# Optimization experiments

Measured on AMD Instinct MI355X. Metric: run time of the kernel, lower is better.

Reference implementation:

```python
import jax, jax.numpy as jnp
import numpy as np

ROWS, CELLS = 64, 64          # B table rows, C cells per row
CN_LEN, CV_LEN = 8, 16        # tokens per column name / cell value
EMB, HID = 768, 3072
VOCAB, NTYPES = 32000, 8
N = ROWS * CELLS              # total cells
L_CV = CELLS * CV_LEN         # padded per-row cv length (max possible)


def setup_inputs() -> dict:
    key = jax.random.key(0)
    ks = jax.random.split(key, 12)
    cn_ids = jax.random.randint(ks[0], (N, CN_LEN), 0, VOCAB)
    # guarantee at least one valid token per column name (avoid div by zero)
    cn_mask = jax.random.randint(ks[1], (N, CN_LEN), 0, 2).at[:, 0].set(1)
    c_types = jax.random.randint(ks[2], (N,), 0, NTYPES)
    cv_ids = jax.random.randint(ks[3], (N, CV_LEN), 0, VOCAB)
    cv_mask = jax.random.randint(ks[4], (N, CV_LEN), 0, 2).astype(bool)
    s = 1.0 / np.sqrt(EMB)
    word_emb = jax.random.normal(ks[5], (VOCAB, EMB), jnp.float32) * 0.02
    type_emb = jax.random.normal(ks[6], (NTYPES, EMB), jnp.float32) * 0.02
    fuse_w1 = jax.random.normal(ks[7], (EMB, HID), jnp.float32) * s
    fuse_b1 = jnp.zeros((HID,), jnp.float32)
    fuse_w2 = jax.random.normal(ks[8], (HID, 1), jnp.float32) / np.sqrt(HID)
    fuse_b2 = jnp.zeros((1,), jnp.float32)
    gate_w1 = jax.random.normal(ks[9], (EMB, HID), jnp.float32) * s
    gate_b1 = jnp.zeros((HID,), jnp.float32)
    gate_w2 = jax.random.normal(ks[10], (HID, 1), jnp.float32) / np.sqrt(HID)
    gate_b2 = jnp.zeros((1,), jnp.float32)
    cls_weight = jax.random.uniform(ks[11], (1, 1, EMB), jnp.float32, -s, s)
    return dict(cn_ids=cn_ids, cn_mask=cn_mask, c_types=c_types, cv_ids=cv_ids,
                cv_mask=cv_mask, word_emb=word_emb, type_emb=type_emb,
                fuse_w1=fuse_w1, fuse_b1=fuse_b1, fuse_w2=fuse_w2, fuse_b2=fuse_b2,
                gate_w1=gate_w1, gate_b1=gate_b1, gate_w2=gate_w2, gate_b2=gate_b2,
                cls_weight=cls_weight)


def reference(cn_ids, cn_mask, c_types, cv_ids, cv_mask, word_emb, type_emb,
              fuse_w1, fuse_b1, fuse_w2, fuse_b2, gate_w1, gate_b1, gate_w2,
              gate_b2, cls_weight):
    # --- TabColumnEmb: masked avg of column-name tokens + datatype gate ---
    cn_we = word_emb[cn_ids]                                  # [N, cn_len, E]
    m = cn_mask.astype(cn_we.dtype)
    cn_e = (cn_we * m[..., None]).sum(1) / m.sum(1, keepdims=True)  # [N, E]
    dt_e = type_emb[c_types]                                  # [N, E]
    fgate = jax.nn.sigmoid(jax.nn.relu(dt_e @ fuse_w1 + fuse_b1) @ fuse_w2 + fuse_b2)
    cn_e = cn_e + dt_e * fgate
    # --- TabColumnValueEmb + RelationLink ---
    cv_e = word_emb[cv_ids]                                   # [N, cv_len, E]
    g = jax.nn.sigmoid(jax.nn.relu(cn_e @ gate_w1 + gate_b1) @ gate_w2 + gate_b2)
    linked = cv_e + (cn_e * g)[:, None, :]                    # [N, cv_len, E]
    # --- per-row ragged gather of masked cv tokens, zero-padded to L_CV ---
    cn_rows = cn_e.reshape(ROWS, CELLS, EMB)
    cv_rows = linked.reshape(ROWS, L_CV, EMB)
    mrows = cv_mask.reshape(ROWS, L_CV)
    pos = jnp.clip(jnp.cumsum(mrows.astype(jnp.int32), axis=1) - 1, 0, L_CV - 1)
    bidx = jnp.arange(ROWS)[:, None]
    mf = mrows[..., None].astype(cv_rows.dtype)
    # masked-out tokens contribute exact zeros -> pad_zeros semantics preserved
    cv_out = jnp.zeros((ROWS, L_CV, EMB), cv_rows.dtype).at[bidx, pos].add(cv_rows * mf)
    # --- TabCLSEmb: prepend learnable cls token ---
    cls = jnp.broadcast_to(cls_weight, (ROWS, 1, EMB))
    return jnp.concatenate([cls, cn_rows, cv_out], axis=1)    # [B, 1+C+L_CV, E]
```

## Files before the change

### kernel.cpp

```cpp
#include <hip/hip_runtime.h>
#include <hip/hip_bf16.h>

#define ROWS 64
#define CELLS 64
#define CN_LEN 8
#define CV_LEN 16
#define EMB 768
#define HID 3072
#define NCELL 4096
#define L_CV 1024
#define ROW_TOK 1089
#define HBLK 24

#define OFF_FPART 0UL
#define OFF_FGATE (OFF_FPART + 96UL*8*4)
#define OFF_GPART (OFF_FGATE + 64UL)
#define OFF_CNB   (OFF_GPART + 24UL*4096*4)
#define OFF_W1T   (OFF_CNB + 4096UL*768*2)
#define OFF_CST   (OFF_W1T + 3072UL*768*2)
#define OFF_CNT   (OFF_CST + 4096UL*4)

typedef __attribute__((ext_vector_type(8))) short bf16x8;
typedef __attribute__((ext_vector_type(4))) float f32x4;

static __device__ __forceinline__ short f2bf(float x) {
  unsigned u = __float_as_uint(x);
  unsigned r = (u + 0x7fffu + ((u >> 16) & 1u)) >> 16;
  return (short)r;
}

static __device__ __forceinline__ void gload16(const void* g, void* l) {
  __builtin_amdgcn_global_load_lds(
      (const __attribute__((address_space(1))) unsigned*)g,
      (__attribute__((address_space(3))) unsigned*)l, 16, 0, 0);
}

__global__ __launch_bounds__(512) void k_fgate_acc(
    const float* __restrict__ type_emb, const float* __restrict__ fuse_w1,
    const float* __restrict__ fuse_b1, const float* __restrict__ fuse_w2,
    float* __restrict__ fpart) {
  __shared__ float te[8 * EMB];
  __shared__ float red[16][8][33];
  const int tid = threadIdx.x;
  for (int i = tid; i < 8 * EMB; i += 512) te[i] = type_emb[i];
  __syncthreads();
  const int hl = tid & 31, eg = tid >> 5;
  const int h = blockIdx.x * 32 + hl;
  float acc[8] = {0.f, 0.f, 0.f, 0.f, 0.f, 0.f, 0.f, 0.f};
  const float* wp = fuse_w1 + h;
  #pragma unroll 4
  for (int i = 0; i < 48; i++) {
    const int e = eg * 48 + i;
    const float wv = wp[(size_t)e * HID];
    #pragma unroll
    for (int t = 0; t < 8; t++) acc[t] += te[t * EMB + e] * wv;
  }
  #pragma unroll
  for (int t = 0; t < 8; t++) red[eg][t][hl] = acc[t];
  __syncthreads();
  if (tid < 256) {
    const int t = tid >> 5, h2 = tid & 31;
    float a = fuse_b1[blockIdx.x * 32 + h2];
    #pragma unroll
    for (int e2 = 0; e2 < 16; e2++) a += red[e2][t][h2];
    float v = fmaxf(a, 0.f) * fuse_w2[blockIdx.x * 32 + h2];
    #pragma unroll
    for (int m = 1; m < 32; m <<= 1) v += __shfl_xor(v, m);
    if (h2 == 0) fpart[blockIdx.x * 8 + t] = v;
  }
}

__global__ __launch_bounds__(256) void k_w1t(const float* __restrict__ w1,
                                             short* __restrict__ w1t,
                                             const float* __restrict__ fpart,
                                             const float* __restrict__ fuse_b2,
                                             float* __restrict__ fgate) {
  __shared__ float tile[32][33];
  const int bx = blockIdx.x, by = blockIdx.y;
  const int tid = threadIdx.x;
  if (bx == 0 && by == 0 && tid < 8) {
    float s = fuse_b2[0];
    for (int j = 0; j < 96; j++) s += fpart[j * 8 + tid];
    fgate[tid] = 1.f / (1.f + expf(-s));
  }
  #pragma unroll
  for (int i = 0; i < 4; i++) {
    int idx = tid + i * 256;
    int rr = idx >> 5, cc = idx & 31;
    tile[rr][cc] = w1[(size_t)(by * 32 + rr) * HID + bx * 32 + cc];
  }
  __syncthreads();
  #pragma unroll
  for (int i = 0; i < 4; i++) {
    int idx = tid + i * 256;
    int rr = idx >> 5, cc = idx & 31;
    w1t[(size_t)(bx * 32 + rr) * EMB + by * 32 + cc] = f2bf(tile[cc][rr]);
  }
}

__global__ __launch_bounds__(192) void k_cn(
    const int* __restrict__ cn_ids, const int* __restrict__ cn_mask,
    const int* __restrict__ c_types, const float* __restrict__ word_emb,
    const float* __restrict__ type_emb, const float* __restrict__ cls_w,
    const float* __restrict__ fgate, short* __restrict__ cnb,
    float* __restrict__ out) {
  const int n = blockIdx.x, tid = threadIdx.x;
  const int row = n >> 6, cell = n & 63;
  const int* ids = cn_ids + n * CN_LEN;
  const int* msk = cn_mask + n * CN_LEN;
  float4 s = {0.f, 0.f, 0.f, 0.f};
  int cnt = 0;
  #pragma unroll
  for (int j = 0; j < CN_LEN; j++) {
    if (msk[j]) {
      cnt++;
      const float4 v = *(const float4*)&word_emb[(size_t)ids[j] * EMB + tid * 4];
      s.x += v.x; s.y += v.y; s.z += v.z; s.w += v.w;
    }
  }
  const float inv = 1.f / (float)cnt;
  const int t = c_types[n];
  const float fg = fgate[t];
  const float4 d = *(const float4*)&type_emb[(size_t)t * EMB + tid * 4];
  float4 c;
  c.x = s.x * inv + d.x * fg;
  c.y = s.y * inv + d.y * fg;
  c.z = s.z * inv + d.z * fg;
  c.w = s.w * inv + d.w * fg;
  short4 b;
  b.x = f2bf(c.x); b.y = f2bf(c.y); b.z = f2bf(c.z); b.w = f2bf(c.w);
  *(short4*)&cnb[(size_t)n * EMB + tid * 4] = b;
  *(float4*)&out[(size_t)row * ROW_TOK * EMB + (size_t)(1 + cell) * EMB + tid * 4] = c;
  if (cell == 0)
    *(float4*)&out[(size_t)row * ROW_TOK * EMB + tid * 4] =
        *(const float4*)&cls_w[tid * 4];
}

__global__ __launch_bounds__(512) void k_gate_gemm(
    const short* __restrict__ cnb, const short* __restrict__ w1t,
    const float* __restrict__ gate_b1, const float* __restrict__ gate_w2,
    float* __restrict__ gpart) {
  __shared__ short Asub[256 * 32];
  __shared__ short Bsub[128 * 32];
  const int tid = threadIdx.x;
  const int n0 = blockIdx.x * 256;
  const int h0 = blockIdx.y * 128;
  const int lane = tid & 63, w = tid >> 6;
  const int wr = w >> 1, wc = w & 1;
  const int r = lane & 15, g = lane >> 4;
  f32x4 acc[4][4];
  #pragma unroll
  for (int a = 0; a < 4; a++)
    #pragma unroll
    for (int b = 0; b < 4; b++) acc[a][b] = (f32x4)0.f;

  const int s0 = tid, s1 = tid + 512;
  const int ar0 = s0 >> 2, ac0 = (s0 & 3) * 8;
  const int ar1 = s1 >> 2, ac1 = (s1 & 3) * 8;

  for (int kk = 0; kk < EMB; kk += 32) {
    gload16(cnb + (size_t)(n0 + ar0) * EMB + kk + ac0, Asub + s0 * 8);
    gload16(cnb + (size_t)(n0 + ar1) * EMB + kk + ac1, Asub + s1 * 8);
    gload16(w1t + (size_t)(h0 + ar0) * EMB + kk + ac0, Bsub + s0 * 8);
    __syncthreads();
    bf16x8 fa[4], fb[4];
    #pragma unroll
    for (int fm = 0; fm < 4; fm++)
      fa[fm] = *(const bf16x8*)&Asub[(wr * 64 + fm * 16 + r) * 32 + g * 8];
    #pragma unroll
    for (int fn = 0; fn < 4; fn++)
      fb[fn] = *(const bf16x8*)&Bsub[(wc * 64 + fn * 16 + r) * 32 + g * 8];
    #pragma unroll
    for (int fm = 0; fm < 4; fm++)
      #pragma unroll
      for (int fn = 0; fn < 4; fn++)
        acc[fm][fn] = __builtin_amdgcn_mfma_f32_16x16x32_bf16(
            fa[fm], fb[fn], acc[fm][fn], 0, 0, 0);
    __syncthreads();
  }

  float rsum[4][4];
  #pragma unroll
  for (int fm = 0; fm < 4; fm++) {
    float rs[4] = {0.f, 0.f, 0.f, 0.f};
    #pragma unroll
    for (int fn = 0; fn < 4; fn++) {
      const int h = h0 + wc * 64 + fn * 16 + r;
      const float bv = gate_b1[h];
      const float wv = gate_w2[h];
      #pragma unroll
      for (int q = 0; q < 4; q++)
        rs[q] += fmaxf(acc[fm][fn][q] + bv, 0.f) * wv;
    }
    #pragma unroll
    for (int q = 0; q < 4; q++) {
      #pragma unroll
      for (int m = 1; m < 16; m <<= 1) rs[q] += __shfl_xor(rs[q], m);
      rsum[fm][q] = rs[q];
    }
  }
  float* red = (float*)Asub;
  __syncthreads();
  if (wc == 1 && r == 0) {
    #pragma unroll
    for (int fm = 0; fm < 4; fm++)
      #pragma unroll
      for (int q = 0; q < 4; q++)
        red[wr * 64 + fm * 16 + g * 4 + q] = rsum[fm][q];
  }
  __syncthreads();
  if (wc == 0 && r == 0) {
    #pragma unroll
    for (int fm = 0; fm < 4; fm++)
      #pragma unroll
      for (int q = 0; q < 4; q++) {
        const int i = wr * 64 + fm * 16 + g * 4 + q;
        gpart[(size_t)blockIdx.y * NCELL + n0 + i] = rsum[fm][q] + red[i];
      }
  }
}

__global__ __launch_bounds__(256) void k_prefix(const int* __restrict__ cv_mask,
                                                int* __restrict__ cstart,
                                                int* __restrict__ cnt) {
  const int row = blockIdx.x, tid = threadIdx.x;
  __shared__ int ssum[256];
  int m[4];
  const int base = row * L_CV + tid * 4;
  int s = 0;
  #pragma unroll
  for (int i = 0; i < 4; i++) { m[i] = cv_mask[base + i]; s += m[i]; }
  ssum[tid] = s;
  __syncthreads();
  for (int off = 1; off < 256; off <<= 1) {
    int v = (tid >= off) ? ssum[tid - off] : 0;
    __syncthreads();
    ssum[tid] += v;
    __syncthreads();
  }
  if ((tid & 3) == 0) cstart[row * CELLS + (tid >> 2)] = ssum[tid] - s;
  if (tid == 255) cnt[row] = ssum[255];
}

__global__ __launch_bounds__(192) void k_cv_cell(
    const int* __restrict__ cv_ids, const int* __restrict__ cv_mask,
    const int* __restrict__ cstart, const int* __restrict__ cnt,
    const float* __restrict__ word_emb, const float* __restrict__ gpart,
    const float* __restrict__ gate_b2, float* __restrict__ out) {
  const int bx = blockIdx.x, row = blockIdx.y, tid = threadIdx.x;
  const size_t rbase = (size_t)row * ROW_TOK * EMB;
  if (bx >= CELLS) {
    const int base = cnt[row] + (bx - CELLS) * 8;
    const float4 z = {0.f, 0.f, 0.f, 0.f};
    #pragma unroll
    for (int i = 0; i < 8; i++) {
      const int k = base + i;
      if (k < L_CV)
        *(float4*)&out[rbase + (size_t)(65 + k) * EMB + tid * 4] = z;
    }
    return;
  }
  const int cell = bx;
  const int n = row * CELLS + cell;
  float sg = gate_b2[0];
  #pragma unroll
  for (int j = 0; j < HBLK; j++) sg += gpart[(size_t)j * NCELL + n];
  const float gg = 1.f / (1.f + expf(-sg));
  const float4 cn = *(const float4*)&out[rbase + (size_t)(1 + cell) * EMB + tid * 4];
  float4 cg;
  cg.x = cn.x * gg; cg.y = cn.y * gg; cg.z = cn.z * gg; cg.w = cn.w * gg;
  const int* ids = cv_ids + n * CV_LEN;
  const int* msk = cv_mask + n * CV_LEN;
  int pos = cstart[n];
  #pragma unroll
  for (int j = 0; j < CV_LEN; j++) {
    if (msk[j]) {
      const float4 we = *(const float4*)&word_emb[(size_t)ids[j] * EMB + tid * 4];
      float4 v;
      v.x = we.x + cg.x; v.y = we.y + cg.y; v.z = we.z + cg.z; v.w = we.w + cg.w;
      *(float4*)&out[rbase + (size_t)(65 + pos) * EMB + tid * 4] = v;
      pos++;
    }
  }
}

extern "C" void kernel_launch(void* const* d_in, const int* in_sizes, int n_in,
                              void* d_out, int out_size, void* d_ws, size_t ws_size,
                              hipStream_t stream) {
  const int* cn_ids    = (const int*)d_in[0];
  const int* cn_mask   = (const int*)d_in[1];
  const int* c_types   = (const int*)d_in[2];
  const int* cv_ids    = (const int*)d_in[3];
  const int* cv_mask   = (const int*)d_in[4];
  const float* word_emb = (const float*)d_in[5];
  const float* type_emb = (const float*)d_in[6];
  const float* fuse_w1  = (const float*)d_in[7];
  const float* fuse_b1  = (const float*)d_in[8];
  const float* fuse_w2  = (const float*)d_in[9];
  const float* fuse_b2  = (const float*)d_in[10];
  const float* gate_w1  = (const float*)d_in[11];
  const float* gate_b1  = (const float*)d_in[12];
  const float* gate_w2  = (const float*)d_in[13];
  const float* gate_b2  = (const float*)d_in[14];
  const float* cls_w    = (const float*)d_in[15];

  char* ws = (char*)d_ws;
  float* fpart = (float*)(ws + OFF_FPART);
  float* fgate = (float*)(ws + OFF_FGATE);
  float* gpart = (float*)(ws + OFF_GPART);
  short* cnb   = (short*)(ws + OFF_CNB);
  short* w1t   = (short*)(ws + OFF_W1T);
  int*   cst   = (int*)(ws + OFF_CST);
  int*   cntp  = (int*)(ws + OFF_CNT);
  float* out   = (float*)d_out;

  k_fgate_acc<<<96, 512, 0, stream>>>(type_emb, fuse_w1, fuse_b1, fuse_w2, fpart);
  k_w1t<<<dim3(96, 24), 256, 0, stream>>>(gate_w1, w1t, fpart, fuse_b2, fgate);
  k_cn<<<NCELL, 192, 0, stream>>>(cn_ids, cn_mask, c_types, word_emb, type_emb,
                                  cls_w, fgate, cnb, out);
  k_gate_gemm<<<dim3(16, HBLK), 512, 0, stream>>>(cnb, w1t, gate_b1, gate_w2, gpart);
  k_prefix<<<64, 256, 0, stream>>>(cv_mask, cst, cntp);
  k_cv_cell<<<dim3(CELLS + 128, ROWS), 192, 0, stream>>>(cv_ids, cv_mask, cst,
                                                         cntp, word_emb, gpart,
                                                         gate_b2, out);
}
```

Measured before the change: 125.2 us.

## Double-buffer gate GEMM, retile to 128x128 with XCD remap, fold prefix into fgate

```diff
diff --git a/kernel.cpp b/kernel.cpp
--- a/kernel.cpp
+++ b/kernel.cpp
@@ -38,10 +38,29 @@
 __global__ __launch_bounds__(512) void k_fgate_acc(
     const float* __restrict__ type_emb, const float* __restrict__ fuse_w1,
     const float* __restrict__ fuse_b1, const float* __restrict__ fuse_w2,
-    float* __restrict__ fpart) {
+    float* __restrict__ fpart, const int* __restrict__ cv_mask,
+    int* __restrict__ cstart, int* __restrict__ cnt) {
   __shared__ float te[8 * EMB];
   __shared__ float red[16][8][33];
+  __shared__ int ssum[512];
   const int tid = threadIdx.x;
+  if (blockIdx.x >= 96) {
+    const int row = blockIdx.x - 96;
+    const int base = row * L_CV + tid * 2;
+    const int m0 = cv_mask[base], m1 = cv_mask[base + 1];
+    const int s = m0 + m1;
+    ssum[tid] = s;
+    __syncthreads();
+    for (int off = 1; off < 512; off <<= 1) {
+      int v = (tid >= off) ? ssum[tid - off] : 0;
+      __syncthreads();
+      ssum[tid] += v;
+      __syncthreads();
+    }
+    if ((tid & 7) == 0) cstart[row * CELLS + (tid >> 3)] = ssum[tid] - s;
+    if (tid == 511) cnt[row] = ssum[511];
+    return;
+  }
   for (int i = tid; i < 8 * EMB; i += 512) te[i] = type_emb[i];
   __syncthreads();
   const int hl = tid & 31, eg = tid >> 5;
@@ -136,15 +155,17 @@
         *(const float4*)&cls_w[tid * 4];
 }
 
-__global__ __launch_bounds__(512) void k_gate_gemm(
+__global__ __launch_bounds__(256) void k_gate_gemm(
     const short* __restrict__ cnb, const short* __restrict__ w1t,
     const float* __restrict__ gate_b1, const float* __restrict__ gate_w2,
     float* __restrict__ gpart) {
-  __shared__ short Asub[256 * 32];
-  __shared__ short Bsub[128 * 32];
+  __shared__ short Asub[2][128 * 32];
+  __shared__ short Bsub[2][128 * 32];
   const int tid = threadIdx.x;
-  const int n0 = blockIdx.x * 256;
-  const int h0 = blockIdx.y * 128;
+  const int orig = blockIdx.x;
+  const int wgid = (orig & 7) * 96 + (orig >> 3);
+  const int bx = wgid & 31, by = wgid >> 5;
+  const int n0 = bx * 128, h0 = by * 128;
   const int lane = tid & 63, w = tid >> 6;
   const int wr = w >> 1, wc = w & 1;
   const int r = lane & 15, g = lane >> 4;
@@ -154,30 +175,47 @@
     #pragma unroll
     for (int b = 0; b < 4; b++) acc[a][b] = (f32x4)0.f;
 
-  const int s0 = tid, s1 = tid + 512;
+  const int s0 = tid, s1 = tid + 256;
   const int ar0 = s0 >> 2, ac0 = (s0 & 3) * 8;
   const int ar1 = s1 >> 2, ac1 = (s1 & 3) * 8;
-
-  for (int kk = 0; kk < EMB; kk += 32) {
-    gload16(cnb + (size_t)(n0 + ar0) * EMB + kk + ac0, Asub + s0 * 8);
-    gload16(cnb + (size_t)(n0 + ar1) * EMB + kk + ac1, Asub + s1 * 8);
-    gload16(w1t + (size_t)(h0 + ar0) * EMB + kk + ac0, Bsub + s0 * 8);
+  const short* aB = cnb + (size_t)n0 * EMB;
+  const short* bB = w1t + (size_t)h0 * EMB;
+
+#define STAGE(buf, kk)                                                  \
+  do {                                                                  \
+    gload16(aB + (size_t)ar0 * EMB + (kk) + ac0, &Asub[buf][s0 * 8]);   \
+    gload16(aB + (size_t)ar1 * EMB + (kk) + ac1, &Asub[buf][s1 * 8]);   \
+    gload16(bB + (size_t)ar0 * EMB + (kk) + ac0, &Bsub[buf][s0 * 8]);   \
+    gload16(bB + (size_t)ar1 * EMB + (kk) + ac1, &Bsub[buf][s1 * 8]);   \
+  } while (0)
+
+#define COMPUTE(buf)                                                          \
+  do {                                                                        \
+    bf16x8 fa[4], fb[4];                                                      \
+    _Pragma("unroll")                                                         \
+    for (int fm = 0; fm < 4; fm++)                                            \
+      fa[fm] = *(const bf16x8*)&Asub[buf][(wr * 64 + fm * 16 + r) * 32 + g * 8]; \
+    _Pragma("unroll")                                                         \
+    for (int fn = 0; fn < 4; fn++)                                            \
+      fb[fn] = *(const bf16x8*)&Bsub[buf][(wc * 64 + fn * 16 + r) * 32 + g * 8]; \
+    _Pragma("unroll")                                                         \
+    for (int fm = 0; fm < 4; fm++)                                            \
+      _Pragma("unroll")                                                       \
+      for (int fn = 0; fn < 4; fn++)                                          \
+        acc[fm][fn] = __builtin_amdgcn_mfma_f32_16x16x32_bf16(                \
+            fa[fm], fb[fn], acc[fm][fn], 0, 0, 0);                            \
+  } while (0)
+
+  STAGE(0, 0);
+  __syncthreads();
+  int cur = 0;
+  for (int t = 0; t < 23; t++) {
+    STAGE(cur ^ 1, (t + 1) * 32);
+    COMPUTE(cur);
     __syncthreads();
-    bf16x8 fa[4], fb[4];
-    #pragma unroll
-    for (int fm = 0; fm < 4; fm++)
-      fa[fm] = *(const bf16x8*)&Asub[(wr * 64 + fm * 16 + r) * 32 + g * 8];
-    #pragma unroll
-    for (int fn = 0; fn < 4; fn++)
-      fb[fn] = *(const bf16x8*)&Bsub[(wc * 64 + fn * 16 + r) * 32 + g * 8];
-    #pragma unroll
-    for (int fm = 0; fm < 4; fm++)
-      #pragma unroll
-      for (int fn = 0; fn < 4; fn++)
-        acc[fm][fn] = __builtin_amdgcn_mfma_f32_16x16x32_bf16(
-            fa[fm], fb[fn], acc[fm][fn], 0, 0, 0);
-    __syncthreads();
-  }
+    cur ^= 1;
+  }
+  COMPUTE(cur);
 
   float rsum[4][4];
   #pragma unroll
@@ -199,7 +237,7 @@
       rsum[fm][q] = rs[q];
     }
   }
-  float* red = (float*)Asub;
+  float* red = (float*)&Asub[0][0];
   __syncthreads();
   if (wc == 1 && r == 0) {
     #pragma unroll
@@ -215,31 +253,11 @@
       #pragma unroll
       for (int q = 0; q < 4; q++) {
         const int i = wr * 64 + fm * 16 + g * 4 + q;
-        gpart[(size_t)blockIdx.y * NCELL + n0 + i] = rsum[fm][q] + red[i];
+        gpart[(size_t)by * NCELL + n0 + i] = rsum[fm][q] + red[i];
       }
   }
-}
-
-__global__ __launch_bounds__(256) void k_prefix(const int* __restrict__ cv_mask,
-                                                int* __restrict__ cstart,
-                                                int* __restrict__ cnt) {
-  const int row = blockIdx.x, tid = threadIdx.x;
-  __shared__ int ssum[256];
-  int m[4];
-  const int base = row * L_CV + tid * 4;
-  int s = 0;
-  #pragma unroll
-  for (int i = 0; i < 4; i++) { m[i] = cv_mask[base + i]; s += m[i]; }
-  ssum[tid] = s;
-  __syncthreads();
-  for (int off = 1; off < 256; off <<= 1) {
-    int v = (tid >= off) ? ssum[tid - off] : 0;
-    __syncthreads();
-    ssum[tid] += v;
-    __syncthreads();
-  }
-  if ((tid & 3) == 0) cstart[row * CELLS + (tid >> 2)] = ssum[tid] - s;
-  if (tid == 255) cnt[row] = ssum[255];
+#undef STAGE
+#undef COMPUTE
 }
 
 __global__ __launch_bounds__(192) void k_cv_cell(
@@ -314,12 +332,12 @@
   int*   cntp  = (int*)(ws + OFF_CNT);
   float* out   = (float*)d_out;
 
-  k_fgate_acc<<<96, 512, 0, stream>>>(type_emb, fuse_w1, fuse_b1, fuse_w2, fpart);
+  k_fgate_acc<<<160, 512, 0, stream>>>(type_emb, fuse_w1, fuse_b1, fuse_w2,
+                                       fpart, cv_mask, cst, cntp);
   k_w1t<<<dim3(96, 24), 256, 0, stream>>>(gate_w1, w1t, fpart, fuse_b2, fgate);
   k_cn<<<NCELL, 192, 0, stream>>>(cn_ids, cn_mask, c_types, word_emb, type_emb,
                                   cls_w, fgate, cnb, out);
-  k_gate_gemm<<<dim3(16, HBLK), 512, 0, stream>>>(cnb, w1t, gate_b1, gate_w2, gpart);
-  k_prefix<<<64, 256, 0, stream>>>(cv_mask, cst, cntp);
+  k_gate_gemm<<<768, 256, 0, stream>>>(cnb, w1t, gate_b1, gate_w2, gpart);
   k_cv_cell<<<dim3(CELLS + 128, ROWS), 192, 0, stream>>>(cv_ids, cv_mask, cst,
                                                          cntp, word_emb, gpart,
                                                          gate_b2, out);
```

After: 123.3 us. No clear change (-1.6%).

## Fold prefix scan into fgate kernel, inline fgate sum, retile gate GEMM

Applied to the files above, without the earlier changes.

```diff
diff --git a/kernel.cpp b/kernel.cpp
--- a/kernel.cpp
+++ b/kernel.cpp
@@ -13,8 +13,7 @@
 #define HBLK 24
 
 #define OFF_FPART 0UL
-#define OFF_FGATE (OFF_FPART + 96UL*8*4)
-#define OFF_GPART (OFF_FGATE + 64UL)
+#define OFF_GPART (OFF_FPART + 96UL*8*4)
 #define OFF_CNB   (OFF_GPART + 24UL*4096*4)
 #define OFF_W1T   (OFF_CNB + 4096UL*768*2)
 #define OFF_CST   (OFF_W1T + 3072UL*768*2)
@@ -38,10 +37,29 @@
 __global__ __launch_bounds__(512) void k_fgate_acc(
     const float* __restrict__ type_emb, const float* __restrict__ fuse_w1,
     const float* __restrict__ fuse_b1, const float* __restrict__ fuse_w2,
-    float* __restrict__ fpart) {
+    float* __restrict__ fpart, const int* __restrict__ cv_mask,
+    int* __restrict__ cstart, int* __restrict__ cnt) {
   __shared__ float te[8 * EMB];
   __shared__ float red[16][8][33];
+  __shared__ int ssum[512];
   const int tid = threadIdx.x;
+  if (blockIdx.x >= 96) {
+    const int row = blockIdx.x - 96;
+    const int base = row * L_CV + tid * 2;
+    const int m0 = cv_mask[base], m1 = cv_mask[base + 1];
+    const int s = m0 + m1;
+    ssum[tid] = s;
+    __syncthreads();
+    for (int off = 1; off < 512; off <<= 1) {
+      int v = (tid >= off) ? ssum[tid - off] : 0;
+      __syncthreads();
+      ssum[tid] += v;
+      __syncthreads();
+    }
+    if ((tid & 7) == 0) cstart[row * CELLS + (tid >> 3)] = ssum[tid] - s;
+    if (tid == 511) cnt[row] = ssum[511];
+    return;
+  }
   for (int i = tid; i < 8 * EMB; i += 512) te[i] = type_emb[i];
   __syncthreads();
   const int hl = tid & 31, eg = tid >> 5;
@@ -71,18 +89,10 @@
 }
 
 __global__ __launch_bounds__(256) void k_w1t(const float* __restrict__ w1,
-                                             short* __restrict__ w1t,
-                                             const float* __restrict__ fpart,
-                                             const float* __restrict__ fuse_b2,
-                                             float* __restrict__ fgate) {
+                                             short* __restrict__ w1t) {
   __shared__ float tile[32][33];
   const int bx = blockIdx.x, by = blockIdx.y;
   const int tid = threadIdx.x;
-  if (bx == 0 && by == 0 && tid < 8) {
-    float s = fuse_b2[0];
-    for (int j = 0; j < 96; j++) s += fpart[j * 8 + tid];
-    fgate[tid] = 1.f / (1.f + expf(-s));
-  }
   #pragma unroll
   for (int i = 0; i < 4; i++) {
     int idx = tid + i * 256;
@@ -102,8 +112,8 @@
     const int* __restrict__ cn_ids, const int* __restrict__ cn_mask,
     const int* __restrict__ c_types, const float* __restrict__ word_emb,
     const float* __restrict__ type_emb, const float* __restrict__ cls_w,
-    const float* __restrict__ fgate, short* __restrict__ cnb,
-    float* __restrict__ out) {
+    const float* __restrict__ fpart, const float* __restrict__ fuse_b2,
+    short* __restrict__ cnb, float* __restrict__ out) {
   const int n = blockIdx.x, tid = threadIdx.x;
   const int row = n >> 6, cell = n & 63;
   const int* ids = cn_ids + n * CN_LEN;
@@ -120,7 +130,10 @@
   }
   const float inv = 1.f / (float)cnt;
   const int t = c_types[n];
-  const float fg = fgate[t];
+  float sg = fuse_b2[0];
+  #pragma unroll 8
+  for (int j = 0; j < 96; j++) sg += fpart[j * 8 + t];
+  const float fg = 1.f / (1.f + expf(-sg));
   const float4 d = *(const float4*)&type_emb[(size_t)t * EMB + tid * 4];
   float4 c;
   c.x = s.x * inv + d.x * fg;
@@ -136,42 +149,49 @@
         *(const float4*)&cls_w[tid * 4];
 }
 
-__global__ __launch_bounds__(512) void k_gate_gemm(
+__global__ __launch_bounds__(256) void k_gate_gemm(
     const short* __restrict__ cnb, const short* __restrict__ w1t,
     const float* __restrict__ gate_b1, const float* __restrict__ gate_w2,
     float* __restrict__ gpart) {
   __shared__ short Asub[256 * 32];
   __shared__ short Bsub[128 * 32];
   const int tid = threadIdx.x;
-  const int n0 = blockIdx.x * 256;
-  const int h0 = blockIdx.y * 128;
+  const int orig = blockIdx.x;
+  const int wgid = (orig & 7) * 48 + (orig >> 3);
+  const int bx = wgid & 15, by = wgid >> 4;
+  const int n0 = bx * 256, h0 = by * 128;
   const int lane = tid & 63, w = tid >> 6;
   const int wr = w >> 1, wc = w & 1;
   const int r = lane & 15, g = lane >> 4;
-  f32x4 acc[4][4];
-  #pragma unroll
-  for (int a = 0; a < 4; a++)
+  f32x4 acc[8][4];
+  #pragma unroll
+  for (int a = 0; a < 8; a++)
     #pragma unroll
     for (int b = 0; b < 4; b++) acc[a][b] = (f32x4)0.f;
 
-  const int s0 = tid, s1 = tid + 512;
-  const int ar0 = s0 >> 2, ac0 = (s0 & 3) * 8;
-  const int ar1 = s1 >> 2, ac1 = (s1 & 3) * 8;
+  const int ar = tid >> 2, ac = (tid & 3) * 8;
+  const short* aB = cnb + (size_t)n0 * EMB;
+  const short* bB = w1t + (size_t)h0 * EMB;
 
   for (int kk = 0; kk < EMB; kk += 32) {
-    gload16(cnb + (size_t)(n0 + ar0) * EMB + kk + ac0, Asub + s0 * 8);
-    gload16(cnb + (size_t)(n0 + ar1) * EMB + kk + ac1, Asub + s1 * 8);
-    gload16(w1t + (size_t)(h0 + ar0) * EMB + kk + ac0, Bsub + s0 * 8);
+    #pragma unroll
+    for (int i = 0; i < 4; i++)
+      gload16(aB + (size_t)(ar + i * 64) * EMB + kk + ac,
+              Asub + (ar + i * 64) * 32 + ac);
+    #pragma unroll
+    for (int i = 0; i < 2; i++)
+      gload16(bB + (size_t)(ar + i * 64) * EMB + kk + ac,
+              Bsub + (ar + i * 64) * 32 + ac);
     __syncthreads();
-    bf16x8 fa[4], fb[4];
-    #pragma unroll
-    for (int fm = 0; fm < 4; fm++)
-      fa[fm] = *(const bf16x8*)&Asub[(wr * 64 + fm * 16 + r) * 32 + g * 8];
+    bf16x8 fa[8], fb[4];
+    #pragma unroll
+    for (int fm = 0; fm < 8; fm++)
+      fa[fm] = *(const bf16x8*)&Asub[(wr * 128 + fm * 16 + r) * 32 + g * 8];
     #pragma unroll
     for (int fn = 0; fn < 4; fn++)
       fb[fn] = *(const bf16x8*)&Bsub[(wc * 64 + fn * 16 + r) * 32 + g * 8];
     #pragma unroll
-    for (int fm = 0; fm < 4; fm++)
+    for (int fm = 0; fm < 8; fm++)
       #pragma unroll
       for (int fn = 0; fn < 4; fn++)
         acc[fm][fn] = __builtin_amdgcn_mfma_f32_16x16x32_bf16(
@@ -179,9 +199,9 @@
     __syncthreads();
   }
 
-  float rsum[4][4];
-  #pragma unroll
-  for (int fm = 0; fm < 4; fm++) {
+  float rsum[8][4];
+  #pragma unroll
+  for (int fm = 0; fm < 8; fm++) {
     float rs[4] = {0.f, 0.f, 0.f, 0.f};
     #pragma unroll
     for (int fn = 0; fn < 4; fn++) {
@@ -203,43 +223,21 @@
   __syncthreads();
   if (wc == 1 && r == 0) {
     #pragma unroll
-    for (int fm = 0; fm < 4; fm++)
+    for (int fm = 0; fm < 8; fm++)
       #pragma unroll
       for (int q = 0; q < 4; q++)
-        red[wr * 64 + fm * 16 + g * 4 + q] = rsum[fm][q];
+        red[wr * 128 + fm * 16 + g * 4 + q] = rsum[fm][q];
   }
   __syncthreads();
   if (wc == 0 && r == 0) {
     #pragma unroll
-    for (int fm = 0; fm < 4; fm++)
+    for (int fm = 0; fm < 8; fm++)
       #pragma unroll
       for (int q = 0; q < 4; q++) {
-        const int i = wr * 64 + fm * 16 + g * 4 + q;
-        gpart[(size_t)blockIdx.y * NCELL + n0 + i] = rsum[fm][q] + red[i];
+        const int i = wr * 128 + fm * 16 + g * 4 + q;
+        gpart[(size_t)by * NCELL + n0 + i] = rsum[fm][q] + red[i];
       }
   }
-}
-
-__global__ __launch_bounds__(256) void k_prefix(const int* __restrict__ cv_mask,
-                                                int* __restrict__ cstart,
-                                                int* __restrict__ cnt) {
-  const int row = blockIdx.x, tid = threadIdx.x;
-  __shared__ int ssum[256];
-  int m[4];
-  const int base = row * L_CV + tid * 4;
-  int s = 0;
-  #pragma unroll
-  for (int i = 0; i < 4; i++) { m[i] = cv_mask[base + i]; s += m[i]; }
-  ssum[tid] = s;
-  __syncthreads();
-  for (int off = 1; off < 256; off <<= 1) {
-    int v = (tid >= off) ? ssum[tid - off] : 0;
-    __syncthreads();
-    ssum[tid] += v;
-    __syncthreads();
-  }
-  if ((tid & 3) == 0) cstart[row * CELLS + (tid >> 2)] = ssum[tid] - s;
-  if (tid == 255) cnt[row] = ssum[255];
 }
 
 __global__ __launch_bounds__(192) void k_cv_cell(
@@ -306,7 +304,6 @@
 
   char* ws = (char*)d_ws;
   float* fpart = (float*)(ws + OFF_FPART);
-  float* fgate = (float*)(ws + OFF_FGATE);
   float* gpart = (float*)(ws + OFF_GPART);
   short* cnb   = (short*)(ws + OFF_CNB);
   short* w1t   = (short*)(ws + OFF_W1T);
@@ -314,12 +311,12 @@
   int*   cntp  = (int*)(ws + OFF_CNT);
   float* out   = (float*)d_out;
 
-  k_fgate_acc<<<96, 512, 0, stream>>>(type_emb, fuse_w1, fuse_b1, fuse_w2, fpart);
-  k_w1t<<<dim3(96, 24), 256, 0, stream>>>(gate_w1, w1t, fpart, fuse_b2, fgate);
+  k_fgate_acc<<<160, 512, 0, stream>>>(type_emb, fuse_w1, fuse_b1, fuse_w2,
+                                       fpart, cv_mask, cst, cntp);
+  k_w1t<<<dim3(96, 24), 256, 0, stream>>>(gate_w1, w1t);
   k_cn<<<NCELL, 192, 0, stream>>>(cn_ids, cn_mask, c_types, word_emb, type_emb,
-                                  cls_w, fgate, cnb, out);
-  k_gate_gemm<<<dim3(16, HBLK), 512, 0, stream>>>(cnb, w1t, gate_b1, gate_w2, gpart);
-  k_prefix<<<64, 256, 0, stream>>>(cv_mask, cst, cntp);
+                                  cls_w, fpart, fuse_b2, cnb, out);
+  k_gate_gemm<<<384, 256, 0, stream>>>(cnb, w1t, gate_b1, gate_w2, gpart);
   k_cv_cell<<<dim3(CELLS + 128, ROWS), 192, 0, stream>>>(cv_ids, cv_mask, cst,
                                                          cntp, word_emb, gpart,
                                                          gate_b2, out);
```

After: 153.8 us. 1.23x slower.
